# Optimization experiments

Measured on AMD Instinct MI355X. Metric: run time of the kernel, lower is better.

Reference implementation:

```python
import jax, jax.numpy as jnp
import numpy as np

H = 1024      # hidden_size
NH = 16       # num_heads
HD = H // NH  # head_dim = 64
BUCKETS = 256
MAXREL = 512
SPAN = BUCKETS  # pos_ebd_size (position_buckets > 0)
B, S = 2, 2048


def setup_inputs() -> dict:
    key = jax.random.key(0)
    ks = jax.random.split(key, 10)
    s = 0.02
    return {
        'hidden_states': jax.random.normal(ks[0], (B, S, H), jnp.float32),
        'Wq': jax.random.normal(ks[1], (H, H), jnp.float32) * s, 'bq': jnp.zeros((H,), jnp.float32),
        'Wk': jax.random.normal(ks[2], (H, H), jnp.float32) * s, 'bk': jnp.zeros((H,), jnp.float32),
        'Wv': jax.random.normal(ks[3], (H, H), jnp.float32) * s, 'bv': jnp.zeros((H,), jnp.float32),
        'Wo': jax.random.normal(ks[4], (H, H), jnp.float32) * s, 'bo': jnp.zeros((H,), jnp.float32),
        'Wpk': jax.random.normal(ks[5], (H, H), jnp.float32) * s, 'bpk': jnp.zeros((H,), jnp.float32),
        'Wpq': jax.random.normal(ks[6], (H, H), jnp.float32) * s, 'bpq': jnp.zeros((H,), jnp.float32),
        'rel_emb': jax.random.normal(ks[7], (2 * SPAN, H), jnp.float32) * s,
        'ln_g': jnp.ones((H,), jnp.float32), 'ln_b': jnp.zeros((H,), jnp.float32),
    }


def _log_bucket(rel, bucket_size, max_position):
    # Faithful port of make_log_bucket_position
    sign = jnp.sign(rel).astype(jnp.float32)
    mid = bucket_size // 2
    abs_pos = jnp.where((rel < mid) & (rel > -mid), mid - 1, jnp.abs(rel)).astype(jnp.float32)
    log_pos = jnp.ceil(jnp.log(abs_pos / mid) / np.float32(np.log((max_position - 1) / mid)) * (mid - 1)) + mid
    bucket = jnp.where(abs_pos <= mid, rel.astype(jnp.float32), log_pos * sign)
    return bucket.astype(jnp.int32)


def _split_heads(x, b, s):
    # [B,S,H] -> [B,NH,S,HD]
    return x.reshape(b, s, NH, HD).transpose(0, 2, 1, 3)


def reference(hidden_states, Wq, bq, Wk, bk, Wv, bv, Wo, bo, Wpk, bpk, Wpq, bpq, rel_emb, ln_g, ln_b):
    b, s, _ = hidden_states.shape
    q = _split_heads(hidden_states @ Wq + bq, b, s)
    k = _split_heads(hidden_states @ Wk + bk, b, s)
    v = _split_heads(hidden_states @ Wv + bv, b, s)
    # scale_factor = 1 + ('c2p') + ('p2c') = 3
    scale = jnp.sqrt(jnp.asarray(HD * 3, jnp.float32))
    scores = jnp.einsum('bhqd,bhkd->bhqk', q, k) / scale
    # log-bucketed relative positions [S, S]
    ids = jnp.arange(s)
    rel = _log_bucket(ids[:, None] - ids[None, :], BUCKETS, MAXREL)
    # LayerNorm over rel embeddings (biased variance, eps=1e-5)
    mu = rel_emb.mean(-1, keepdims=True)
    var = rel_emb.var(-1, keepdims=True)
    re = (rel_emb - mu) / jnp.sqrt(var + 1e-5) * ln_g + ln_b   # [2*SPAN, H]
    pos_k = (re @ Wpk + bpk).reshape(2 * SPAN, NH, HD).transpose(1, 0, 2)  # [NH, 2*SPAN, HD]
    pos_q = (re @ Wpq + bpq).reshape(2 * SPAN, NH, HD).transpose(1, 0, 2)
    # c2p: content->position
    c2p = jnp.einsum('bhqd,hpd->bhqp', q, pos_k)                 # [B,NH,S,2*SPAN]
    c2p_idx = jnp.clip(rel + SPAN, 0, 2 * SPAN - 1)              # [S,S]
    c2p = jnp.take_along_axis(c2p, jnp.broadcast_to(c2p_idx[None, None], (b, NH, s, s)), axis=-1) / scale
    # p2c: position->content (gather on key axis, then transpose)
    p2c = jnp.einsum('bhkd,hpd->bhkp', k, pos_q)                 # [B,NH,S,2*SPAN]
    p2c_idx = jnp.clip(-rel + SPAN, 0, 2 * SPAN - 1)
    p2c = jnp.take_along_axis(p2c, jnp.broadcast_to(p2c_idx[None, None], (b, NH, s, s)), axis=-1)
    p2c = jnp.swapaxes(p2c, -1, -2) / scale
    scores = scores + c2p + p2c
    probs = jax.nn.softmax(scores.astype(jnp.float32), axis=-1).astype(q.dtype)
    ctx = jnp.einsum('bhqk,bhkd->bhqd', probs, v)
    ctx = ctx.transpose(0, 2, 1, 3).reshape(b, s, H)
    return ctx @ Wo + bo
```

## Files before the change

### kernel.cpp

```cpp
#include <hip/hip_runtime.h>

typedef unsigned short u16;
typedef __attribute__((ext_vector_type(8))) short short8;
typedef __attribute__((ext_vector_type(4))) float float4v;

#define MFMA16(a, b, c) __builtin_amdgcn_mfma_f32_16x16x32_bf16((a), (b), (c), 0, 0, 0)

__device__ __forceinline__ u16 f2b(float x) {
    union { float f; unsigned u; } v; v.f = x;
    unsigned r = v.u + 0x7FFFu + ((v.u >> 16) & 1u);
    return (u16)(r >> 16);
}
__device__ __forceinline__ float b2f(u16 u) {
    union { unsigned u; float f; } v; v.u = ((unsigned)u) << 16; return v.f;
}

#define NH 16
#define S  2048
#define HD 64
#define H  1024
#define SC 0.10412111829775301f

#define OFF_REB   0ull
#define OFF_HSB   (OFF_REB  + 1048576ull)
#define OFF_WT    (OFF_HSB  + 8388608ull)
#define OFF_QB    (OFF_WT   + 12582912ull)
#define OFF_KB    (OFF_QB   + 8388608ull)
#define OFF_VT    (OFF_KB   + 8388608ull)
#define OFF_PKB   (OFF_VT   + 8388608ull)
#define OFF_PQB   (OFF_PKB  + 1048576ull)
#define OFF_C2P   (OFF_PQB  + 1048576ull)
#define OFF_P2CT  (OFF_C2P  + 67108864ull)
#define OFF_CTX   (OFF_P2CT + 67108864ull)
#define OFF_IDX   (OFF_CTX  + 8388608ull)
#define OFF_SP    (OFF_IDX  + 8192ull)
#define SP_OHALF  4194304ull
#define SP_LBASE  (OFF_SP + 67108864ull)
#define SP_LHALF  65536ull
#define WS_NEED_SPLIT (SP_LBASE + 524288ull)

__global__ void k_build_idx(short* __restrict__ t) {
    int i = blockIdx.x * 256 + threadIdx.x;
    if (i >= 1024) return;
    int rel = i - 512;
    float fr = (float)rel;
    float abs_pos = (rel < 128 && rel > -128) ? 127.0f : fabsf(fr);
    const float LOGC = 1.3843393262841284f;
    float log_pos = ceilf(logf(abs_pos * (1.0f / 128.0f)) / LOGC * 127.0f) + 128.0f;
    float sgn = (fr > 0.f) ? 1.f : ((fr < 0.f) ? -1.f : 0.f);
    float bf = (abs_pos <= 128.0f) ? fr : log_pos * sgn;
    int idx = (int)bf + 256;
    idx = idx < 0 ? 0 : (idx > 511 ? 511 : idx);
    t[i] = (short)idx;
}

__global__ __launch_bounds__(256) void k_ln(const float* __restrict__ re,
                                            const float* __restrict__ g,
                                            const float* __restrict__ be,
                                            u16* __restrict__ out) {
    int row = blockIdx.x;
    const float4* x4 = (const float4*)(re + (size_t)row * H);
    int tid = threadIdx.x;
    float4 vv = x4[tid];
    float s = vv.x + vv.y + vv.z + vv.w;
    float s2 = vv.x * vv.x + vv.y * vv.y + vv.z * vv.z + vv.w * vv.w;
    for (int m = 1; m < 64; m <<= 1) {
        s += __shfl_xor(s, m, 64);
        s2 += __shfl_xor(s2, m, 64);
    }
    __shared__ float as[4], as2[4];
    if ((tid & 63) == 0) { as[tid >> 6] = s; as2[tid >> 6] = s2; }
    __syncthreads();
    s = as[0] + as[1] + as[2] + as[3];
    s2 = as2[0] + as2[1] + as2[2] + as2[3];
    float mu = s * (1.f / 1024.f);
    float var = s2 * (1.f / 1024.f) - mu * mu;
    float rstd = rsqrtf(var + 1e-5f);
    float4 gg = ((const float4*)g)[tid];
    float4 bb = ((const float4*)be)[tid];
    ushort4 r4;
    r4.x = f2b((vv.x - mu) * rstd * gg.x + bb.x);
    r4.y = f2b((vv.y - mu) * rstd * gg.y + bb.y);
    r4.z = f2b((vv.z - mu) * rstd * gg.z + bb.z);
    r4.w = f2b((vv.w - mu) * rstd * gg.w + bb.w);
    ((ushort4*)(out + (size_t)row * H))[tid] = r4;
}

__global__ __launch_bounds__(256) void k_cast(const float* __restrict__ x, u16* __restrict__ y) {
    int i = blockIdx.x * 256 + threadIdx.x;
    float4 v = ((const float4*)x)[i];
    ushort4 r;
    r.x = f2b(v.x); r.y = f2b(v.y); r.z = f2b(v.z); r.w = f2b(v.w);
    ((ushort4*)y)[i] = r;
}

__global__ __launch_bounds__(256) void k_wt6(const float* __restrict__ W0, const float* __restrict__ W1,
                                             const float* __restrict__ W2, const float* __restrict__ W3,
                                             const float* __restrict__ W4, const float* __restrict__ W5,
                                             u16* __restrict__ T0, u16* __restrict__ T1,
                                             u16* __restrict__ T2, u16* __restrict__ T3,
                                             u16* __restrict__ T4, u16* __restrict__ T5) {
    const float* W; u16* WT;
    switch (blockIdx.z) {
        case 0: W = W0; WT = T0; break;
        case 1: W = W1; WT = T1; break;
        case 2: W = W2; WT = T2; break;
        case 3: W = W3; WT = T3; break;
        case 4: W = W4; WT = T4; break;
        default: W = W5; WT = T5; break;
    }
    __shared__ float t[64][65];
    int k0 = blockIdx.x * 64, n0 = blockIdx.y * 64;
    int tid = threadIdx.x;
#pragma unroll
    for (int i = 0; i < 16; i++) {
        int lin = tid + 256 * i;
        int r = lin >> 6, c = lin & 63;
        t[r][c] = W[(size_t)(k0 + r) * H + n0 + c];
    }
    __syncthreads();
#pragma unroll
    for (int i = 0; i < 16; i++) {
        int lin = tid + 256 * i;
        int r = lin >> 6, c = lin & 63;
        WT[(size_t)(n0 + r) * H + k0 + c] = f2b(t[c][r]);
    }
}

template <int MODE>
__device__ __forceinline__ void gemm2_body(const u16* __restrict__ A,
                                           const u16* __restrict__ Bt,
                                           const float* __restrict__ bias,
                                           void* __restrict__ C, int N, int K) {
    __shared__ __align__(16) u16 As[128 * 32];
    __shared__ __align__(16) u16 Bs[128 * 32];
    int tid = threadIdx.x;
    int lane = tid & 63, w = tid >> 6;
    int ln = lane & 15, quad = lane >> 4;
    int m0 = blockIdx.x * 128, n0 = blockIdx.y * 128;
    int wm = (w >> 1) * 64, wn = (w & 1) * 64;
    float4v acc[4][4];
    float4v zero = {0.f, 0.f, 0.f, 0.f};
#pragma unroll
    for (int mi = 0; mi < 4; mi++)
#pragma unroll
        for (int ni = 0; ni < 4; ni++) acc[mi][ni] = zero;

    int r1 = tid >> 2, o1 = (tid & 3) * 8;
    const u16* ga1 = A + (size_t)(m0 + r1) * K + o1;
    const u16* gb1 = Bt + (size_t)(n0 + r1) * K + o1;
    u16* sa1 = &As[r1 * 32 + o1];
    u16* sb1 = &Bs[r1 * 32 + o1];
    size_t step2 = (size_t)64 * K;

    for (int k0 = 0; k0 < K; k0 += 32) {
        short8 va1 = *(const short8*)(ga1 + k0);
        short8 va2 = *(const short8*)(ga1 + step2 + k0);
        short8 vb1 = *(const short8*)(gb1 + k0);
        short8 vb2 = *(const short8*)(gb1 + step2 + k0);
        __syncthreads();
        *(short8*)sa1 = va1; *(short8*)(sa1 + 2048) = va2;
        *(short8*)sb1 = vb1; *(short8*)(sb1 + 2048) = vb2;
        __syncthreads();
        short8 af[4], bf[4];
#pragma unroll
        for (int mi = 0; mi < 4; mi++)
            af[mi] = *(const short8*)&As[(wm + mi * 16 + ln) * 32 + quad * 8];
#pragma unroll
        for (int ni = 0; ni < 4; ni++)
            bf[ni] = *(const short8*)&Bs[(wn + ni * 16 + ln) * 32 + quad * 8];
#pragma unroll
        for (int mi = 0; mi < 4; mi++)
#pragma unroll
            for (int ni = 0; ni < 4; ni++)
                acc[mi][ni] = MFMA16(af[mi], bf[ni], acc[mi][ni]);
    }

#pragma unroll
    for (int mi = 0; mi < 4; mi++) {
        int row0 = m0 + wm + mi * 16 + quad * 4;
#pragma unroll
        for (int ni = 0; ni < 4; ni++) {
            int col = n0 + wn + ni * 16 + ln;
            float bv = bias[col];
            if (MODE == 0) {
                u16* Cb = (u16*)C;
#pragma unroll
                for (int r = 0; r < 4; r++)
                    Cb[(size_t)(row0 + r) * N + col] = f2b(acc[mi][ni][r] + bv);
            } else if (MODE == 1) {
                float* Cf = (float*)C;
#pragma unroll
                for (int r = 0; r < 4; r++)
                    Cf[(size_t)(row0 + r) * N + col] = acc[mi][ni][r] + bv;
            } else if (MODE == 2) {
                u16* Cb = (u16*)C;
                int bb = row0 >> 11, s = row0 & 2047;
                ushort4 r4;
                r4.x = f2b(acc[mi][ni][0] + bv);
                r4.y = f2b(acc[mi][ni][1] + bv);
                r4.z = f2b(acc[mi][ni][2] + bv);
                r4.w = f2b(acc[mi][ni][3] + bv);
                *(ushort4*)(Cb + ((size_t)(bb * 1024 + col)) * 2048 + s) = r4;
            } else {
                u16* Cb = (u16*)C;
                int bb = row0 >> 11, s = row0 & 2047;
                int h = col >> 6, d = col & 63;
#pragma unroll
                for (int r = 0; r < 4; r++)
                    Cb[((size_t)(bb * 16 + h) * 2048 + s + r) * 64 + d] = f2b(acc[mi][ni][r] + bv);
            }
        }
    }
}

template <int MODE>
__global__ __launch_bounds__(256) void k_gemm2(const u16* __restrict__ A, const u16* __restrict__ Bt,
                                               const float* __restrict__ bias, void* __restrict__ C,
                                               int N, int K) {
    gemm2_body<MODE>(A, Bt, bias, C, N, K);
}

template <int MODE>
__global__ __launch_bounds__(256) void k_gemm2_dual(const u16* __restrict__ A,
                                                    const u16* __restrict__ Bt0, const u16* __restrict__ Bt1,
                                                    const float* __restrict__ b0, const float* __restrict__ b1,
                                                    void* __restrict__ C0, void* __restrict__ C1,
                                                    int N, int K) {
    if (blockIdx.z == 0) gemm2_body<MODE>(A, Bt0, b0, C0, N, K);
    else                 gemm2_body<MODE>(A, Bt1, b1, C1, N, K);
}

__global__ __launch_bounds__(256) void k_qkv(const u16* __restrict__ A,
                                             const u16* __restrict__ W0, const u16* __restrict__ W1,
                                             const u16* __restrict__ W2,
                                             const float* __restrict__ b0, const float* __restrict__ b1,
                                             const float* __restrict__ b2,
                                             u16* __restrict__ Q, u16* __restrict__ K, u16* __restrict__ VT) {
    if (blockIdx.z == 0)      gemm2_body<3>(A, W0, b0, Q, H, H);
    else if (blockIdx.z == 1) gemm2_body<3>(A, W1, b1, K, H, H);
    else                      gemm2_body<2>(A, W2, b2, VT, H, H);
}

__global__ __launch_bounds__(256) void k_pos_both(const u16* __restrict__ Qh, const u16* __restrict__ Kh,
                                                  const u16* __restrict__ pk, const u16* __restrict__ pq,
                                                  u16* __restrict__ c2p, u16* __restrict__ p2cT) {
    __shared__ __align__(16) u16 smem[2 * 128 * 72];
    u16* As = smem;
    u16* Bs = smem + 128 * 72;
    int tid = threadIdx.x;
    int lane = tid & 63, w = tid >> 6;
    int ln = lane & 15, quad = lane >> 4;
    int tr = blockIdx.z & 1, z = blockIdx.z >> 1, h = z & 15;
    int m0 = blockIdx.x * 128, n0 = blockIdx.y * 128;
    const u16* A = (tr ? Kh : Qh) + (size_t)z * S * HD;
    const u16* B = (tr ? pq : pk) + h * 64;
    int sr = tid >> 1, scb = (tid & 1) * 32;
    {
        const u16* ga = A + (size_t)(m0 + sr) * HD + scb;
        const u16* gb = B + (size_t)(n0 + sr) * H + scb;
#pragma unroll
        for (int j = 0; j < 4; j++) {
            *(short8*)&As[sr * 72 + scb + j * 8] = *(const short8*)(ga + j * 8);
            *(short8*)&Bs[sr * 72 + scb + j * 8] = *(const short8*)(gb + j * 8);
        }
    }
    __syncthreads();
    int wm = (w >> 1) * 64, wn = (w & 1) * 64;
    float4v acc[4][4];
    float4v zero = {0.f, 0.f, 0.f, 0.f};
#pragma unroll
    for (int mi = 0; mi < 4; mi++)
#pragma unroll
        for (int ni = 0; ni < 4; ni++) acc[mi][ni] = zero;
#pragma unroll
    for (int c = 0; c < 2; c++) {
        short8 af[4], bf[4];
#pragma unroll
        for (int mi = 0; mi < 4; mi++)
            af[mi] = *(const short8*)&As[(wm + mi * 16 + ln) * 72 + c * 32 + quad * 8];
#pragma unroll
        for (int ni = 0; ni < 4; ni++)
            bf[ni] = *(const short8*)&Bs[(wn + ni * 16 + ln) * 72 + c * 32 + quad * 8];
#pragma unroll
        for (int mi = 0; mi < 4; mi++)
#pragma unroll
            for (int ni = 0; ni < 4; ni++)
                acc[mi][ni] = MFMA16(af[mi], bf[ni], acc[mi][ni]);
    }
    if (!tr) {
        u16* Cp = c2p + (size_t)z * S * 512;
#pragma unroll
        for (int mi = 0; mi < 4; mi++) {
            int row0 = m0 + wm + mi * 16 + quad * 4;
#pragma unroll
            for (int ni = 0; ni < 4; ni++) {
                int col = n0 + wn + ni * 16 + ln;
#pragma unroll
                for (int r = 0; r < 4; r++)
                    Cp[(size_t)(row0 + r) * 512 + col] = f2b(acc[mi][ni][r] * SC);
            }
        }
    } else {
        __syncthreads();
        u16* Ts = smem;
#pragma unroll
        for (int mi = 0; mi < 4; mi++) {
            int rl0 = wm + mi * 16 + quad * 4;
#pragma unroll
            for (int ni = 0; ni < 4; ni++) {
                int cl = wn + ni * 16 + ln;
#pragma unroll
                for (int r = 0; r < 4; r++)
                    Ts[cl * 136 + rl0 + r] = f2b(acc[mi][ni][r] * SC);
            }
        }
        __syncthreads();
        u16* Cp = p2cT + (size_t)z * 512 * S;
        int pr = tid >> 1, mb = (tid & 1) * 64;
        u16* dst = Cp + (size_t)(n0 + pr) * S + m0 + mb;
        const u16* src = Ts + pr * 136 + mb;
#pragma unroll
        for (int j = 0; j < 8; j++)
            *(short8*)(dst + j * 8) = *(const short8*)(src + j * 8);
    }
}

template <int SPLIT>
__global__ __launch_bounds__(256, 4) void k_attn(const u16* __restrict__ Qh,
                                                 const u16* __restrict__ Kh,
                                                 const u16* __restrict__ VT,
                                                 const u16* __restrict__ c2p,
                                                 const u16* __restrict__ p2cT,
                                                 const short* __restrict__ idxTab,
                                                 float* __restrict__ oP,
                                                 float* __restrict__ lP,
                                                 u16* __restrict__ ctx) {
    __shared__ short s_idx1[1024];
    __shared__ __align__(16) u16 p_lds[4][16][72];
    __shared__ __align__(16) u16 Ks[64][72];
    __shared__ __align__(16) u16 Vs[64][72];
    int tid = threadIdx.x;
    for (int i = tid; i < 1024; i += 256) s_idx1[i] = idxTab[i];
    int lane = tid & 63, w = tid >> 6;
    int ln = lane & 15, quad = lane >> 4;
    int bx = blockIdx.x;
    int half = (SPLIT == 2) ? (bx & 1) : 0;
    int q0 = (SPLIT == 2) ? (bx >> 1) * 64 : bx * 64;
    int bh = blockIdx.y;
    int b = bh >> 4, h = bh & 15;
    int qs = q0 + w * 16;

    const u16* qptr = Qh + ((size_t)bh * S + qs + ln) * HD + quad * 8;
    short8 aq0 = *(const short8*)(qptr);
    short8 aq1 = *(const short8*)(qptr + 32);

    float4v o[4];
    float4v zero = {0.f, 0.f, 0.f, 0.f};
#pragma unroll
    for (int f = 0; f < 4; f++) o[f] = zero;
    float lrw[4] = {0.f, 0.f, 0.f, 0.f};

    const u16* c2pB = c2p + (size_t)bh * S * 512;
    const u16* p2cB = p2cT + (size_t)bh * 512 * S;
    int qrow = qs + quad * 4;

    int sr = tid >> 2, sc = (tid & 3) * 16;
    const u16* kstg = Kh + ((size_t)bh * S + sr) * HD + sc;
    const u16* vstg = VT + (size_t)(b * 1024 + h * 64 + sr) * S + sc;

    const int NT = S / 64 / SPLIT;
    for (int t = 0; t < NT; t++) {
        int kk = (SPLIT == 2) ? (((t << 1) | half) << 6) : (t << 6);
        short8 kr0 = *(const short8*)(kstg + (size_t)kk * HD);
        short8 kr1 = *(const short8*)(kstg + (size_t)kk * HD + 8);
        short8 vr0 = *(const short8*)(vstg + kk);
        short8 vr1 = *(const short8*)(vstg + kk + 8);
        __syncthreads();
        *(short8*)&Ks[sr][sc] = kr0; *(short8*)&Ks[sr][sc + 8] = kr1;
        *(short8*)&Vs[sr][sc] = vr0; *(short8*)&Vs[sr][sc + 8] = vr1;
        __syncthreads();
        float4v sa[4];
#pragma unroll
        for (int f = 0; f < 4; f++) {
            short8 b0 = *(const short8*)&Ks[f * 16 + ln][quad * 8];
            short8 b1 = *(const short8*)&Ks[f * 16 + ln][32 + quad * 8];
            float4v tt = zero;
            tt = MFMA16(aq0, b0, tt);
            tt = MFMA16(aq1, b1, tt);
            sa[f] = tt;
        }
        int rel0 = q0 - kk;
        if (rel0 >= 569 || rel0 <= -633) {
            int idx = rel0 > 0 ? 511 : 0;
            float cvr[4];
#pragma unroll
            for (int r = 0; r < 4; r++)
                cvr[r] = b2f(c2pB[(size_t)(qrow + r) * 512 + idx]);
            const u16* prow = p2cB + (size_t)idx * S + kk;
#pragma unroll
            for (int f = 0; f < 4; f++) {
                float pv = b2f(prow[f * 16 + ln]);
#pragma unroll
                for (int r = 0; r < 4; r++) {
                    float p = exp2f(sa[f][r] * SC + cvr[r] + pv);
                    lrw[r] += p;
                    p_lds[w][quad * 4 + r][f * 16 + ln] = f2b(p);
                }
            }
        } else {
#pragma unroll
            for (int f = 0; f < 4; f++) {
                int ki = kk + f * 16 + ln;
                int relb = qrow - ki;
#pragma unroll
                for (int r = 0; r < 4; r++) {
                    int rel = relb + r;
                    rel = rel < -512 ? -512 : (rel > 511 ? 511 : rel);
                    int idx = (int)s_idx1[rel + 512];
                    float cv = b2f(c2pB[(size_t)(qrow + r) * 512 + idx]);
                    float pv = b2f(p2cB[(size_t)idx * S + ki]);
                    float p = exp2f(sa[f][r] * SC + cv + pv);
                    lrw[r] += p;
                    p_lds[w][quad * 4 + r][f * 16 + ln] = f2b(p);
                }
            }
        }
        short8 ap0 = *(const short8*)&p_lds[w][ln][quad * 8];
        short8 ap1 = *(const short8*)&p_lds[w][ln][32 + quad * 8];
#pragma unroll
        for (int f = 0; f < 4; f++) {
            short8 v0 = *(const short8*)&Vs[f * 16 + ln][quad * 8];
            short8 v1 = *(const short8*)&Vs[f * 16 + ln][32 + quad * 8];
            o[f] = MFMA16(ap0, v0, o[f]);
            o[f] = MFMA16(ap1, v1, o[f]);
        }
    }
#pragma unroll
    for (int r = 0; r < 4; r++) {
        lrw[r] += __shfl_xor(lrw[r], 1, 16);
        lrw[r] += __shfl_xor(lrw[r], 2, 16);
        lrw[r] += __shfl_xor(lrw[r], 4, 16);
        lrw[r] += __shfl_xor(lrw[r], 8, 16);
    }
    if (SPLIT == 1) {
        float inv_l[4];
#pragma unroll
        for (int r = 0; r < 4; r++) inv_l[r] = 1.f / lrw[r];
#pragma unroll
        for (int f = 0; f < 4; f++)
#pragma unroll
            for (int r = 0; r < 4; r++) {
                int qi = qs + quad * 4 + r;
                ctx[(size_t)(b * S + qi) * H + h * 64 + f * 16 + ln] = f2b(o[f][r] * inv_l[r]);
            }
    } else {
        float* oH = oP + (size_t)half * SP_OHALF;
#pragma unroll
        for (int f = 0; f < 4; f++)
#pragma unroll
            for (int r = 0; r < 4; r++) {
                int qi = qs + quad * 4 + r;
                oH[((size_t)bh * S + qi) * 64 + f * 16 + ln] = o[f][r];
            }
        if (ln == 0) {
            float* lH = lP + (size_t)half * SP_LHALF;
#pragma unroll
            for (int r = 0; r < 4; r++)
                lH[(size_t)bh * S + qs + quad * 4 + r] = lrw[r];
        }
    }
}

__global__ __launch_bounds__(256) void k_merge(const float* __restrict__ oP,
                                               const float* __restrict__ lP,
                                               u16* __restrict__ ctx) {
    int t = blockIdx.x * 256 + threadIdx.x;
    int d4 = (t & 15) * 4;
    int h  = (t >> 4) & 15;
    int qq = (t >> 8) & 2047;
    int b  = t >> 19;
    int bh = b * 16 + h;
    size_t base = ((size_t)bh * S + qq) * 64 + d4;
    float4 o0 = *(const float4*)(oP + base);
    float4 o1 = *(const float4*)(oP + SP_OHALF + base);
    float l0 = lP[(size_t)bh * S + qq];
    float l1 = lP[SP_LHALF + (size_t)bh * S + qq];
    float inv = 1.f / (l0 + l1);
    ushort4 r4;
    r4.x = f2b((o0.x + o1.x) * inv);
    r4.y = f2b((o0.y + o1.y) * inv);
    r4.z = f2b((o0.z + o1.z) * inv);
    r4.w = f2b((o0.w + o1.w) * inv);
    *(ushort4*)(ctx + (((size_t)(b * S + qq)) * 16 + h) * 64 + d4) = r4;
}

extern "C" void kernel_launch(void* const* d_in, const int* in_sizes, int n_in,
                              void* d_out, int out_size, void* d_ws, size_t ws_size,
                              hipStream_t stream) {
    const float* hs  = (const float*)d_in[0];
    const float* Wq  = (const float*)d_in[1];
    const float* bq  = (const float*)d_in[2];
    const float* Wk  = (const float*)d_in[3];
    const float* bk  = (const float*)d_in[4];
    const float* Wv  = (const float*)d_in[5];
    const float* bv  = (const float*)d_in[6];
    const float* Wo  = (const float*)d_in[7];
    const float* bo  = (const float*)d_in[8];
    const float* Wpk = (const float*)d_in[9];
    const float* bpk = (const float*)d_in[10];
    const float* Wpq = (const float*)d_in[11];
    const float* bpq = (const float*)d_in[12];
    const float* rel = (const float*)d_in[13];
    const float* lng = (const float*)d_in[14];
    const float* lnb = (const float*)d_in[15];

    char* ws = (char*)d_ws;
    u16* re_b   = (u16*)(ws + OFF_REB);
    u16* hs_b   = (u16*)(ws + OFF_HSB);
    u16* wt0    = (u16*)(ws + OFF_WT);
    u16* wt1    = (u16*)(ws + OFF_WT + 2097152ull);
    u16* wt2    = (u16*)(ws + OFF_WT + 2ull * 2097152ull);
    u16* wt3    = (u16*)(ws + OFF_WT + 3ull * 2097152ull);
    u16* wt4    = (u16*)(ws + OFF_WT + 4ull * 2097152ull);
    u16* wt5    = (u16*)(ws + OFF_WT + 5ull * 2097152ull);
    u16* Q_b    = (u16*)(ws + OFF_QB);
    u16* K_b    = (u16*)(ws + OFF_KB);
    u16* VT_b   = (u16*)(ws + OFF_VT);
    u16* posk_b = (u16*)(ws + OFF_PKB);
    u16* posq_b = (u16*)(ws + OFF_PQB);
    u16* c2p_b  = (u16*)(ws + OFF_C2P);
    u16* p2cT_b = (u16*)(ws + OFF_P2CT);
    u16* ctx_b  = (u16*)(ws + OFF_CTX);
    short* idx_t = (short*)(ws + OFF_IDX);
    float* oP   = (float*)(ws + OFF_SP);
    float* lP   = (float*)(ws + SP_LBASE);

    dim3 blk(256);
    k_build_idx<<<dim3(4), blk, 0, stream>>>(idx_t);
    k_ln<<<dim3(512), blk, 0, stream>>>(rel, lng, lnb, re_b);
    k_cast<<<dim3(4096), blk, 0, stream>>>(hs, hs_b);
    k_wt6<<<dim3(16, 16, 6), blk, 0, stream>>>(Wq, Wk, Wv, Wo, Wpk, Wpq,
                                               wt0, wt1, wt2, wt3, wt4, wt5);

    k_qkv<<<dim3(32, 8, 3), blk, 0, stream>>>(hs_b, wt0, wt1, wt2, bq, bk, bv, Q_b, K_b, VT_b);
    k_gemm2_dual<0><<<dim3(4, 8, 2), blk, 0, stream>>>(re_b, wt4, wt5, bpk, bpq, posk_b, posq_b, H, H);

    k_pos_both<<<dim3(16, 4, 64), blk, 0, stream>>>(Q_b, K_b, posk_b, posq_b, c2p_b, p2cT_b);

    if (ws_size >= WS_NEED_SPLIT) {
        k_attn<2><<<dim3(64, 32), blk, 0, stream>>>(Q_b, K_b, VT_b, c2p_b, p2cT_b, idx_t, oP, lP, ctx_b);
        k_merge<<<dim3(4096), blk, 0, stream>>>(oP, lP, ctx_b);
    } else {
        k_attn<1><<<dim3(32, 32), blk, 0, stream>>>(Q_b, K_b, VT_b, c2p_b, p2cT_b, idx_t, oP, lP, ctx_b);
    }

    k_gemm2<1><<<dim3(32, 8), blk, 0, stream>>>(ctx_b, wt3, bo, d_out, H, H);
}
```

Before: 402.8 us.

## Store p2c in key-major layout and batch gather loads in attention

The p2c position table is now written key-major ([S,512] per head), the same layout as c2p, instead of transposed ([512,S]). Both k_pos_both outputs now go through a shared LDS-staged path with coalesced 16-byte row writes. In attention, the p2c gather for each key indexes within that key's row, and the four c2p/p2c loads are issued together before the exp, to raise memory-level parallelism. The trade-off is that the bucketed fast path now reads p2c with a 1024-byte stride across lanes instead of contiguous loads along the key axis.

```diff
diff --git a/kernel.cpp b/kernel.cpp
--- a/kernel.cpp
+++ b/kernel.cpp
@@ -30,8 +30,8 @@
 #define OFF_PKB   (OFF_VT   + 8388608ull)
 #define OFF_PQB   (OFF_PKB  + 1048576ull)
 #define OFF_C2P   (OFF_PQB  + 1048576ull)
-#define OFF_P2CT  (OFF_C2P  + 67108864ull)
-#define OFF_CTX   (OFF_P2CT + 67108864ull)
+#define OFF_P2CK  (OFF_C2P  + 67108864ull)
+#define OFF_CTX   (OFF_P2CK + 67108864ull)
 #define OFF_IDX   (OFF_CTX  + 8388608ull)
 #define OFF_SP    (OFF_IDX  + 8192ull)
 #define SP_OHALF  4194304ull
@@ -244,7 +244,7 @@
 
 __global__ __launch_bounds__(256) void k_pos_both(const u16* __restrict__ Qh, const u16* __restrict__ Kh,
                                                   const u16* __restrict__ pk, const u16* __restrict__ pq,
-                                                  u16* __restrict__ c2p, u16* __restrict__ p2cT) {
+                                                  u16* __restrict__ c2p, u16* __restrict__ p2cK) {
     __shared__ __align__(16) u16 smem[2 * 128 * 72];
     u16* As = smem;
     u16* Bs = smem + 128 * 72;
@@ -288,42 +288,27 @@
             for (int ni = 0; ni < 4; ni++)
                 acc[mi][ni] = MFMA16(af[mi], bf[ni], acc[mi][ni]);
     }
-    if (!tr) {
-        u16* Cp = c2p + (size_t)z * S * 512;
-#pragma unroll
-        for (int mi = 0; mi < 4; mi++) {
-            int row0 = m0 + wm + mi * 16 + quad * 4;
-#pragma unroll
-            for (int ni = 0; ni < 4; ni++) {
-                int col = n0 + wn + ni * 16 + ln;
-#pragma unroll
-                for (int r = 0; r < 4; r++)
-                    Cp[(size_t)(row0 + r) * 512 + col] = f2b(acc[mi][ni][r] * SC);
-            }
-        }
-    } else {
-        __syncthreads();
-        u16* Ts = smem;
-#pragma unroll
-        for (int mi = 0; mi < 4; mi++) {
-            int rl0 = wm + mi * 16 + quad * 4;
-#pragma unroll
-            for (int ni = 0; ni < 4; ni++) {
-                int cl = wn + ni * 16 + ln;
-#pragma unroll
-                for (int r = 0; r < 4; r++)
-                    Ts[cl * 136 + rl0 + r] = f2b(acc[mi][ni][r] * SC);
-            }
-        }
-        __syncthreads();
-        u16* Cp = p2cT + (size_t)z * 512 * S;
-        int pr = tid >> 1, mb = (tid & 1) * 64;
-        u16* dst = Cp + (size_t)(n0 + pr) * S + m0 + mb;
-        const u16* src = Ts + pr * 136 + mb;
-#pragma unroll
-        for (int j = 0; j < 8; j++)
-            *(short8*)(dst + j * 8) = *(const short8*)(src + j * 8);
-    }
+    __syncthreads();
+    u16* Ts = smem;
+#pragma unroll
+    for (int mi = 0; mi < 4; mi++) {
+        int rl0 = wm + mi * 16 + quad * 4;
+#pragma unroll
+        for (int ni = 0; ni < 4; ni++) {
+            int cl = wn + ni * 16 + ln;
+#pragma unroll
+            for (int r = 0; r < 4; r++)
+                Ts[(rl0 + r) * 136 + cl] = f2b(acc[mi][ni][r] * SC);
+        }
+    }
+    __syncthreads();
+    u16* Cp = (tr ? p2cK : c2p) + (size_t)z * S * 512;
+    int pr = tid >> 1, cb = (tid & 1) * 64;
+    u16* dst = Cp + (size_t)(m0 + pr) * 512 + n0 + cb;
+    const u16* src = Ts + pr * 136 + cb;
+#pragma unroll
+    for (int j = 0; j < 8; j++)
+        *(short8*)(dst + j * 8) = *(const short8*)(src + j * 8);
 }
 
 template <int SPLIT>
@@ -331,7 +316,7 @@
                                                  const u16* __restrict__ Kh,
                                                  const u16* __restrict__ VT,
                                                  const u16* __restrict__ c2p,
-                                                 const u16* __restrict__ p2cT,
+                                                 const u16* __restrict__ p2cK,
                                                  const short* __restrict__ idxTab,
                                                  float* __restrict__ oP,
                                                  float* __restrict__ lP,
@@ -362,8 +347,12 @@
     float lrw[4] = {0.f, 0.f, 0.f, 0.f};
 
     const u16* c2pB = c2p + (size_t)bh * S * 512;
-    const u16* p2cB = p2cT + (size_t)bh * 512 * S;
+    const u16* p2cB = p2cK + (size_t)bh * S * 512;
     int qrow = qs + quad * 4;
+
+    const u16* cvrow[4];
+#pragma unroll
+    for (int r = 0; r < 4; r++) cvrow[r] = c2pB + (size_t)(qrow + r) * 512;
 
     int sr = tid >> 2, sc = (tid & 3) * 16;
     const u16* kstg = Kh + ((size_t)bh * S + sr) * HD + sc;
@@ -396,11 +385,11 @@
             float cvr[4];
 #pragma unroll
             for (int r = 0; r < 4; r++)
-                cvr[r] = b2f(c2pB[(size_t)(qrow + r) * 512 + idx]);
-            const u16* prow = p2cB + (size_t)idx * S + kk;
+                cvr[r] = b2f(cvrow[r][idx]);
 #pragma unroll
             for (int f = 0; f < 4; f++) {
-                float pv = b2f(prow[f * 16 + ln]);
+                int ki = kk + f * 16 + ln;
+                float pv = b2f(p2cB[(size_t)ki * 512 + idx]);
 #pragma unroll
                 for (int r = 0; r < 4; r++) {
                     float p = exp2f(sa[f][r] * SC + cvr[r] + pv);
@@ -412,15 +401,20 @@
 #pragma unroll
             for (int f = 0; f < 4; f++) {
                 int ki = kk + f * 16 + ln;
+                const u16* pvrow = p2cB + (size_t)ki * 512;
                 int relb = qrow - ki;
+                u16 cvu[4], pvu[4];
 #pragma unroll
                 for (int r = 0; r < 4; r++) {
                     int rel = relb + r;
                     rel = rel < -512 ? -512 : (rel > 511 ? 511 : rel);
                     int idx = (int)s_idx1[rel + 512];
-                    float cv = b2f(c2pB[(size_t)(qrow + r) * 512 + idx]);
-                    float pv = b2f(p2cB[(size_t)idx * S + ki]);
-                    float p = exp2f(sa[f][r] * SC + cv + pv);
+                    cvu[r] = cvrow[r][idx];
+                    pvu[r] = pvrow[idx];
+                }
+#pragma unroll
+                for (int r = 0; r < 4; r++) {
+                    float p = exp2f(sa[f][r] * SC + b2f(cvu[r]) + b2f(pvu[r]));
                     lrw[r] += p;
                     p_lds[w][quad * 4 + r][f * 16 + ln] = f2b(p);
                 }
@@ -530,7 +524,7 @@
     u16* posk_b = (u16*)(ws + OFF_PKB);
     u16* posq_b = (u16*)(ws + OFF_PQB);
     u16* c2p_b  = (u16*)(ws + OFF_C2P);
-    u16* p2cT_b = (u16*)(ws + OFF_P2CT);
+    u16* p2cK_b = (u16*)(ws + OFF_P2CK);
     u16* ctx_b  = (u16*)(ws + OFF_CTX);
     short* idx_t = (short*)(ws + OFF_IDX);
     float* oP   = (float*)(ws + OFF_SP);
@@ -546,13 +540,13 @@
     k_qkv<<<dim3(32, 8, 3), blk, 0, stream>>>(hs_b, wt0, wt1, wt2, bq, bk, bv, Q_b, K_b, VT_b);
     k_gemm2_dual<0><<<dim3(4, 8, 2), blk, 0, stream>>>(re_b, wt4, wt5, bpk, bpq, posk_b, posq_b, H, H);
 
-    k_pos_both<<<dim3(16, 4, 64), blk, 0, stream>>>(Q_b, K_b, posk_b, posq_b, c2p_b, p2cT_b);
+    k_pos_both<<<dim3(16, 4, 64), blk, 0, stream>>>(Q_b, K_b, posk_b, posq_b, c2p_b, p2cK_b);
 
     if (ws_size >= WS_NEED_SPLIT) {
-        k_attn<2><<<dim3(64, 32), blk, 0, stream>>>(Q_b, K_b, VT_b, c2p_b, p2cT_b, idx_t, oP, lP, ctx_b);
+        k_attn<2><<<dim3(64, 32), blk, 0, stream>>>(Q_b, K_b, VT_b, c2p_b, p2cK_b, idx_t, oP, lP, ctx_b);
         k_merge<<<dim3(4096), blk, 0, stream>>>(oP, lP, ctx_b);
     } else {
-        k_attn<1><<<dim3(32, 32), blk, 0, stream>>>(Q_b, K_b, VT_b, c2p_b, p2cT_b, idx_t, oP, lP, ctx_b);
+        k_attn<1><<<dim3(32, 32), blk, 0, stream>>>(Q_b, K_b, VT_b, c2p_b, p2cK_b, idx_t, oP, lP, ctx_b);
     }
 
     k_gemm2<1><<<dim3(32, 8), blk, 0, stream>>>(ctx_b, wt3, bo, d_out, H, H);
```

After: 441.6 us. +9.6%, slower.
